# Kernel tuning notes

Measured on AMD Instinct MI355X. Metric: run time of the kernel, lower is better.

Reference implementation:

```python
import jax, jax.numpy as jnp
import numpy as np


def hadamard_matrix(n):
    # Sylvester construction; n must be a power of 2.
    H = np.array([[1.0]], dtype=np.float32)
    while H.shape[0] < n:
        H = np.block([[H, H], [H, -H]])
    return H


def setup_inputs() -> dict:
    key = jax.random.key(0)
    k1, k2, k3 = jax.random.split(key, 3)
    B, C, Hh, Ww, P = 8, 64, 256, 256, 4
    x = jax.random.normal(k1, (B, C, Hh, Ww), dtype=jnp.float32)
    v = jax.random.uniform(k2, (P, Hh, Ww), dtype=jnp.float32)          # torch.rand init
    T = jax.random.uniform(k3, (P, Hh, Ww), dtype=jnp.float32) / 10.0   # torch.rand/10 init
    return {"x": x, "v": v, "T": T}


def _wht2d(u, Hm, sc):
    # normalized Walsh-Hadamard transform along last two axes (H symmetric)
    u = jnp.einsum('...hw,vw->...hv', u, Hm) * sc   # axis=-1
    u = jnp.einsum('...hv,gh->...gv', u, Hm) * sc   # axis=-2
    return u


def reference(x, v, T):
    n = x.shape[-1]  # 256, power of 2; height_pad==height so no padding
    Hm = jnp.asarray(hadamard_matrix(n), dtype=x.dtype)
    sc = jnp.asarray(1.0 / np.sqrt(n), dtype=x.dtype)
    f2 = _wht2d(x, Hm, sc)                              # (B,C,H,W)
    a = f2[None] * v[:, None, None]                     # (P,B,C,H,W)
    st = jnp.tanh(a) * jax.nn.relu(jnp.abs(a) - jnp.abs(T)[:, None, None])
    f6 = st.sum(axis=0)                                 # (B,C,H,W)
    f8 = _wht2d(f6, Hm, sc)
    return f8 + x                                       # residual=True
```

## Files before the change

kernel.cpp:

```cpp
#include <hip/hip_runtime.h>
#include <hip/hip_fp16.h>


#define NPX   65536
#define NROWS (512 * 256)
#define SC    0.0625f

__device__ __forceinline__ unsigned int h2u(__half2 h) {
  union { __half2 h; unsigned int u; } c; c.h = h; return c.u;
}
__device__ __forceinline__ __half2 u2h(unsigned int u) {
  union { __half2 h; unsigned int u; } c; c.u = u; return c.h;
}

__device__ __forceinline__ void fwht16(float f[16]) {
  #pragma unroll
  for (int d = 1; d < 16; d <<= 1) {
    #pragma unroll
    for (int i = 0; i < 16; ++i) {
      if (!(i & d)) {
        float a = f[i], b = f[i | d];
        f[i]     = a + b;
        f[i | d] = a - b;
      }
    }
  }
}

__device__ __forceinline__ void fwht256_wave(float r[4], int lane) {
  float a0 = r[0] + r[1], b0 = r[0] - r[1];
  float a1 = r[2] + r[3], b1 = r[2] - r[3];
  r[0] = a0 + a1; r[1] = b0 + b1; r[2] = a0 - a1; r[3] = b0 - b1;
  #pragma unroll
  for (int m = 1; m <= 32; m <<= 1) {
    const float s = (lane & m) ? -1.0f : 1.0f;
    #pragma unroll
    for (int j = 0; j < 4; ++j) {
      float t = __shfl_xor(r[j], m);
      r[j] = fmaf(r[j], s, t);
    }
  }
}

__device__ __forceinline__ float g_term(float a, float absT) {
  float e  = __builtin_amdgcn_exp2f(a * 2.8853900817779268f);
  float th = 1.0f - 2.0f * __builtin_amdgcn_rcpf(e + 1.0f);
  float rl = fmaxf(fabsf(a) - absT, 0.0f);
  return th * rl;
}

__global__ __launch_bounds__(256) void k_prep(const float* __restrict__ v,
                                              const float* __restrict__ T,
                                              unsigned int* __restrict__ W2) {
  const int pix = blockIdx.x * 256 + threadIdx.x;
  uint4 w;
  w.x = h2u(__floats2half2_rn(v[0 * NPX + pix] * SC, fabsf(T[0 * NPX + pix])));
  w.y = h2u(__floats2half2_rn(v[1 * NPX + pix] * SC, fabsf(T[1 * NPX + pix])));
  w.z = h2u(__floats2half2_rn(v[2 * NPX + pix] * SC, fabsf(T[2 * NPX + pix])));
  w.w = h2u(__floats2half2_rn(v[3 * NPX + pix] * SC, fabsf(T[3 * NPX + pix])));
  *reinterpret_cast<uint4*>(W2 + 4 * (size_t)pix) = w;
}

__global__ __launch_bounds__(256) void k_rowf(const float* __restrict__ x,
                                              __half* __restrict__ t1) {
  const int lane = threadIdx.x & 63;
  const int wave = blockIdx.x * 4 + (threadIdx.x >> 6);
  const int nw   = gridDim.x * 4;
  for (int row = wave; row < NROWS; row += nw) {
    const float4 xv = *reinterpret_cast<const float4*>(x + (size_t)row * 256 + 4 * lane);
    float r[4] = {xv.x, xv.y, xv.z, xv.w};
    fwht256_wave(r, lane);
    uint2 pk;
    pk.x = h2u(__floats2half2_rn(r[0] * SC, r[1] * SC));
    pk.y = h2u(__floats2half2_rn(r[2] * SC, r[3] * SC));
    *reinterpret_cast<uint2*>(t1 + (size_t)row * 256 + 4 * lane) = pk;
  }
}

__global__ __launch_bounds__(512) void k_mid(__half* __restrict__ t1,
                                             const unsigned int* __restrict__ W2) {
  __shared__ __half S[256 * 64];
  const int tid = threadIdx.x;
  const int plane = blockIdx.x >> 2;
  const int w0    = (blockIdx.x & 3) * 64;
  __half* tp = t1 + (size_t)plane * NPX + w0;

  {
    const int cp = tid & 31;
    const int g  = tid >> 5;
    float fA[16], fB[16];
    #pragma unroll
    for (int k = 0; k < 16; ++k) {
      const unsigned int d =
          *reinterpret_cast<const unsigned int*>(tp + (16 * g + k) * 256 + 2 * cp);
      const float2 e = __half22float2(u2h(d));
      fA[k] = e.x; fB[k] = e.y;
    }
    fwht16(fA); fwht16(fB);
    #pragma unroll
    for (int k = 0; k < 16; ++k)
      *reinterpret_cast<unsigned int*>(&S[(16 * g + k) * 64 + 2 * cp]) =
          h2u(__floats2half2_rn(fA[k], fB[k]));
  }
  __syncthreads();

  {
    const int c   = tid & 63;
    const int grp = tid >> 6;
    float f[16];
    #pragma unroll 1
    for (int s = 0; s < 2; ++s) {
      const int gg = grp + 8 * s;
      #pragma unroll
      for (int a = 0; a < 16; ++a)
        f[a] = __half2float(S[(gg + 16 * a) * 64 + c]);
      fwht16(f);

      #pragma unroll 4
      for (int a = 0; a < 16; ++a) {
        const size_t off = (size_t)((gg + 16 * a) * 256 + w0 + c);
        const uint4 wq = *reinterpret_cast<const uint4*>(W2 + 4 * off);
        const float2 p0 = __half22float2(u2h(wq.x));
        const float2 p1 = __half22float2(u2h(wq.y));
        const float2 p2 = __half22float2(u2h(wq.z));
        const float2 p3 = __half22float2(u2h(wq.w));
        float acc;
        acc  = g_term(f[a] * p0.x, p0.y);
        acc += g_term(f[a] * p1.x, p1.y);
        acc += g_term(f[a] * p2.x, p2.y);
        acc += g_term(f[a] * p3.x, p3.y);
        f[a] = acc;
      }

      fwht16(f);
      #pragma unroll
      for (int a = 0; a < 16; ++a)
        S[(gg + 16 * a) * 64 + c] = __float2half_rn(f[a] * SC);
    }
  }
  __syncthreads();

  {
    const int cp = tid & 31;
    const int g  = tid >> 5;
    float fA[16], fB[16];
    #pragma unroll
    for (int k = 0; k < 16; ++k) {
      const float2 e = __half22float2(
          u2h(*reinterpret_cast<unsigned int*>(&S[(16 * g + k) * 64 + 2 * cp])));
      fA[k] = e.x; fB[k] = e.y;
    }
    fwht16(fA); fwht16(fB);
    #pragma unroll
    for (int k = 0; k < 16; ++k)
      *reinterpret_cast<unsigned int*>(tp + (16 * g + k) * 256 + 2 * cp) =
          h2u(__floats2half2_rn(fA[k], fB[k]));
  }
}

__global__ __launch_bounds__(256) void k_rowb(const __half* __restrict__ t1,
                                              const float* __restrict__ x,
                                              float* __restrict__ out) {
  const int lane = threadIdx.x & 63;
  const int wave = blockIdx.x * 4 + (threadIdx.x >> 6);
  const int nw   = gridDim.x * 4;
  for (int row = wave; row < NROWS; row += nw) {
    const uint2 pk = *reinterpret_cast<const uint2*>(t1 + (size_t)row * 256 + 4 * lane);
    const float2 lo = __half22float2(u2h(pk.x));
    const float2 hi = __half22float2(u2h(pk.y));
    float r[4] = {lo.x, lo.y, hi.x, hi.y};
    fwht256_wave(r, lane);
    const float4 xv = *reinterpret_cast<const float4*>(x + (size_t)row * 256 + 4 * lane);
    float4 o;
    o.x = fmaf(r[0], SC, xv.x);
    o.y = fmaf(r[1], SC, xv.y);
    o.z = fmaf(r[2], SC, xv.z);
    o.w = fmaf(r[3], SC, xv.w);
    *reinterpret_cast<float4*>(out + (size_t)row * 256 + 4 * lane) = o;
  }
}

extern "C" void kernel_launch(void* const* d_in, const int* in_sizes, int n_in,
                              void* d_out, int out_size, void* d_ws, size_t ws_size,
                              hipStream_t stream) {
  const float* x = (const float*)d_in[0];
  const float* v = (const float*)d_in[1];
  const float* T = (const float*)d_in[2];
  float* out = (float*)d_out;
  __half* t1 = (__half*)d_ws;
  unsigned int* W2 = (unsigned int*)((char*)d_ws + (size_t)NROWS * 256 * 2);

  k_prep<<<256, 256, 0, stream>>>(v, T, W2);
  k_rowf<<<2048, 256, 0, stream>>>(x, t1);
  k_mid <<<2048, 512, 0, stream>>>(t1, W2);
  k_rowb<<<2048, 256, 0, stream>>>(t1, x, out);
}
```

Measured before the change: 182.4 us.

## Split column Hadamard into radix-16 stages fused into row-transform kernels

Moves the first radix-16 butterfly stage of the column transform into the row-transform kernels. Each wave now handles 16 rows spaced 256 apart and does the 16-point butterfly in packed half2 registers. The middle kernel drops its shared-memory staging and both barriers, and reads and writes the 16-row groups straight from global memory with per-thread strided half accesses. The aim is to cut LDS traffic and syncs and shrink the middle kernel. In exchange it adds fp16 arithmetic precision loss in the butterflies and uncoalesced 2-byte global accesses in the middle kernel.

Result: faster. 173.4 us (-5.0%).

```diff
diff --git a/kernel.cpp b/kernel.cpp
--- a/kernel.cpp
+++ b/kernel.cpp
@@ -42,6 +42,23 @@
   }
 }
 
+__device__ __forceinline__ void fwht16_h2(__half2 h[16][2]) {
+  #pragma unroll
+  for (int d = 1; d < 16; d <<= 1) {
+    #pragma unroll
+    for (int i = 0; i < 16; ++i) {
+      if (!(i & d)) {
+        __half2 a0 = h[i][0], b0 = h[i | d][0];
+        __half2 a1 = h[i][1], b1 = h[i | d][1];
+        h[i][0]     = __hadd2(a0, b0);
+        h[i | d][0] = __hsub2(a0, b0);
+        h[i][1]     = __hadd2(a1, b1);
+        h[i | d][1] = __hsub2(a1, b1);
+      }
+    }
+  }
+}
+
 __device__ __forceinline__ float g_term(float a, float absT) {
   float e  = __builtin_amdgcn_exp2f(a * 2.8853900817779268f);
   float th = 1.0f - 2.0f * __builtin_amdgcn_rcpf(e + 1.0f);
@@ -61,122 +78,94 @@
   *reinterpret_cast<uint4*>(W2 + 4 * (size_t)pix) = w;
 }
 
-__global__ __launch_bounds__(256) void k_rowf(const float* __restrict__ x,
-                                              __half* __restrict__ t1) {
+__global__ __launch_bounds__(256) void k_f1(const float* __restrict__ x,
+                                            __half* __restrict__ t1) {
   const int lane = threadIdx.x & 63;
-  const int wave = blockIdx.x * 4 + (threadIdx.x >> 6);
-  const int nw   = gridDim.x * 4;
-  for (int row = wave; row < NROWS; row += nw) {
-    const float4 xv = *reinterpret_cast<const float4*>(x + (size_t)row * 256 + 4 * lane);
+  const int G    = blockIdx.x * 4 + (threadIdx.x >> 6);
+  const size_t base = (size_t)G * 16 * 256 + 4 * lane;
+  __half2 h[16][2];
+  #pragma unroll
+  for (int k = 0; k < 16; ++k) {
+    const float4 xv = *reinterpret_cast<const float4*>(x + base + (size_t)k * 256);
     float r[4] = {xv.x, xv.y, xv.z, xv.w};
     fwht256_wave(r, lane);
-    uint2 pk;
-    pk.x = h2u(__floats2half2_rn(r[0] * SC, r[1] * SC));
-    pk.y = h2u(__floats2half2_rn(r[2] * SC, r[3] * SC));
-    *reinterpret_cast<uint2*>(t1 + (size_t)row * 256 + 4 * lane) = pk;
+    h[k][0] = __floats2half2_rn(r[0] * SC, r[1] * SC);
+    h[k][1] = __floats2half2_rn(r[2] * SC, r[3] * SC);
+  }
+  fwht16_h2(h);
+  #pragma unroll
+  for (int k = 0; k < 16; ++k) {
+    uint2 pk; pk.x = h2u(h[k][0]); pk.y = h2u(h[k][1]);
+    *reinterpret_cast<uint2*>(t1 + base + (size_t)k * 256) = pk;
   }
 }
 
-__global__ __launch_bounds__(512) void k_mid(__half* __restrict__ t1,
-                                             const unsigned int* __restrict__ W2) {
-  __shared__ __half S[256 * 64];
-  const int tid = threadIdx.x;
+__global__ __launch_bounds__(512) void k_g(__half* __restrict__ t1,
+                                           const unsigned int* __restrict__ W2) {
+  const int tid   = threadIdx.x;
   const int plane = blockIdx.x >> 2;
   const int w0    = (blockIdx.x & 3) * 64;
-  __half* tp = t1 + (size_t)plane * NPX + w0;
+  const int c     = tid & 63;
+  const int grp   = tid >> 6;
+  __half* tp = t1 + (size_t)plane * NPX + w0 + c;
+  float f[16];
+  #pragma unroll 1
+  for (int s = 0; s < 2; ++s) {
+    const int gg = grp + 8 * s;
+    #pragma unroll
+    for (int a = 0; a < 16; ++a)
+      f[a] = __half2float(tp[(gg + 16 * a) * 256]);
+    fwht16(f);
 
-  {
-    const int cp = tid & 31;
-    const int g  = tid >> 5;
-    float fA[16], fB[16];
+    #pragma unroll 4
+    for (int a = 0; a < 16; ++a) {
+      const size_t off = (size_t)((gg + 16 * a) * 256 + w0 + c);
+      const uint4 wq = *reinterpret_cast<const uint4*>(W2 + 4 * off);
+      const float2 p0 = __half22float2(u2h(wq.x));
+      const float2 p1 = __half22float2(u2h(wq.y));
+      const float2 p2 = __half22float2(u2h(wq.z));
+      const float2 p3 = __half22float2(u2h(wq.w));
+      float acc;
+      acc  = g_term(f[a] * p0.x, p0.y);
+      acc += g_term(f[a] * p1.x, p1.y);
+      acc += g_term(f[a] * p2.x, p2.y);
+      acc += g_term(f[a] * p3.x, p3.y);
+      f[a] = acc;
+    }
+
+    fwht16(f);
     #pragma unroll
-    for (int k = 0; k < 16; ++k) {
-      const unsigned int d =
-          *reinterpret_cast<const unsigned int*>(tp + (16 * g + k) * 256 + 2 * cp);
-      const float2 e = __half22float2(u2h(d));
-      fA[k] = e.x; fB[k] = e.y;
-    }
-    fwht16(fA); fwht16(fB);
-    #pragma unroll
-    for (int k = 0; k < 16; ++k)
-      *reinterpret_cast<unsigned int*>(&S[(16 * g + k) * 64 + 2 * cp]) =
-          h2u(__floats2half2_rn(fA[k], fB[k]));
-  }
-  __syncthreads();
-
-  {
-    const int c   = tid & 63;
-    const int grp = tid >> 6;
-    float f[16];
-    #pragma unroll 1
-    for (int s = 0; s < 2; ++s) {
-      const int gg = grp + 8 * s;
-      #pragma unroll
-      for (int a = 0; a < 16; ++a)
-        f[a] = __half2float(S[(gg + 16 * a) * 64 + c]);
-      fwht16(f);
-
-      #pragma unroll 4
-      for (int a = 0; a < 16; ++a) {
-        const size_t off = (size_t)((gg + 16 * a) * 256 + w0 + c);
-        const uint4 wq = *reinterpret_cast<const uint4*>(W2 + 4 * off);
-        const float2 p0 = __half22float2(u2h(wq.x));
-        const float2 p1 = __half22float2(u2h(wq.y));
-        const float2 p2 = __half22float2(u2h(wq.z));
-        const float2 p3 = __half22float2(u2h(wq.w));
-        float acc;
-        acc  = g_term(f[a] * p0.x, p0.y);
-        acc += g_term(f[a] * p1.x, p1.y);
-        acc += g_term(f[a] * p2.x, p2.y);
-        acc += g_term(f[a] * p3.x, p3.y);
-        f[a] = acc;
-      }
-
-      fwht16(f);
-      #pragma unroll
-      for (int a = 0; a < 16; ++a)
-        S[(gg + 16 * a) * 64 + c] = __float2half_rn(f[a] * SC);
-    }
-  }
-  __syncthreads();
-
-  {
-    const int cp = tid & 31;
-    const int g  = tid >> 5;
-    float fA[16], fB[16];
-    #pragma unroll
-    for (int k = 0; k < 16; ++k) {
-      const float2 e = __half22float2(
-          u2h(*reinterpret_cast<unsigned int*>(&S[(16 * g + k) * 64 + 2 * cp])));
-      fA[k] = e.x; fB[k] = e.y;
-    }
-    fwht16(fA); fwht16(fB);
-    #pragma unroll
-    for (int k = 0; k < 16; ++k)
-      *reinterpret_cast<unsigned int*>(tp + (16 * g + k) * 256 + 2 * cp) =
-          h2u(__floats2half2_rn(fA[k], fB[k]));
+    for (int a = 0; a < 16; ++a)
+      tp[(gg + 16 * a) * 256] = __float2half_rn(f[a] * SC);
   }
 }
 
-__global__ __launch_bounds__(256) void k_rowb(const __half* __restrict__ t1,
-                                              const float* __restrict__ x,
-                                              float* __restrict__ out) {
+__global__ __launch_bounds__(256) void k_f3(const __half* __restrict__ t1,
+                                            const float* __restrict__ x,
+                                            float* __restrict__ out) {
   const int lane = threadIdx.x & 63;
-  const int wave = blockIdx.x * 4 + (threadIdx.x >> 6);
-  const int nw   = gridDim.x * 4;
-  for (int row = wave; row < NROWS; row += nw) {
-    const uint2 pk = *reinterpret_cast<const uint2*>(t1 + (size_t)row * 256 + 4 * lane);
-    const float2 lo = __half22float2(u2h(pk.x));
-    const float2 hi = __half22float2(u2h(pk.y));
+  const int G    = blockIdx.x * 4 + (threadIdx.x >> 6);
+  const size_t base = (size_t)G * 16 * 256 + 4 * lane;
+  __half2 h[16][2];
+  #pragma unroll
+  for (int k = 0; k < 16; ++k) {
+    const uint2 pk = *reinterpret_cast<const uint2*>(t1 + base + (size_t)k * 256);
+    h[k][0] = u2h(pk.x); h[k][1] = u2h(pk.y);
+  }
+  fwht16_h2(h);
+  #pragma unroll
+  for (int k = 0; k < 16; ++k) {
+    const float2 lo = __half22float2(h[k][0]);
+    const float2 hi = __half22float2(h[k][1]);
     float r[4] = {lo.x, lo.y, hi.x, hi.y};
     fwht256_wave(r, lane);
-    const float4 xv = *reinterpret_cast<const float4*>(x + (size_t)row * 256 + 4 * lane);
+    const float4 xv = *reinterpret_cast<const float4*>(x + base + (size_t)k * 256);
     float4 o;
     o.x = fmaf(r[0], SC, xv.x);
     o.y = fmaf(r[1], SC, xv.y);
     o.z = fmaf(r[2], SC, xv.z);
     o.w = fmaf(r[3], SC, xv.w);
-    *reinterpret_cast<float4*>(out + (size_t)row * 256 + 4 * lane) = o;
+    *reinterpret_cast<float4*>(out + base + (size_t)k * 256) = o;
   }
 }
 
@@ -191,7 +180,7 @@
   unsigned int* W2 = (unsigned int*)((char*)d_ws + (size_t)NROWS * 256 * 2);
 
   k_prep<<<256, 256, 0, stream>>>(v, T, W2);
-  k_rowf<<<2048, 256, 0, stream>>>(x, t1);
-  k_mid <<<2048, 512, 0, stream>>>(t1, W2);
-  k_rowb<<<2048, 256, 0, stream>>>(t1, x, out);
+  k_f1 <<<2048, 256, 0, stream>>>(x, t1);
+  k_g  <<<2048, 512, 0, stream>>>(t1, W2);
+  k_f3 <<<2048, 256, 0, stream>>>(t1, x, out);
 }
```
